# Optimization experiments

Hardware: AMD Instinct MI355X
Metric: run time of the kernel (lower is better)

Reference implementation:

```python
import jax, jax.numpy as jnp
import numpy as np

N_NODES = 100000
IN_CH = 256
OUT_CH = 128
N_EDGES = 3200000
SCALING_FACTOR = 1.8


def gcn_propagate(x, edge_index, num_nodes):
    """APPNP(K=1, alpha=0) == one step of D^-1/2 (A+I) D^-1/2 @ x."""
    row, col = edge_index[0], edge_index[1]
    loops = jnp.arange(num_nodes, dtype=edge_index.dtype)
    row = jnp.concatenate([row, loops])
    col = jnp.concatenate([col, loops])
    ones = jnp.ones(row.shape[0], dtype=x.dtype)
    deg = jax.ops.segment_sum(ones, col, num_segments=num_nodes)  # [N]
    dinv = jnp.where(deg > 0, jax.lax.rsqrt(deg), 0.0)
    norm = dinv[row] * dinv[col]  # [E+N]
    msgs = x[row] * norm[:, None]  # gather + scale, [E+N, C]
    return jax.ops.segment_sum(msgs, col, num_segments=num_nodes)  # [N, C]


def setup_inputs() -> dict:
    key = jax.random.key(0)
    ks = jax.random.split(key, 7)
    x = jax.random.normal(ks[0], (N_NODES, IN_CH), dtype=jnp.float32)
    edge_index = jax.random.randint(ks[1], (2, N_EDGES), 0, N_NODES, dtype=jnp.int64)
    s1 = 1.0 / np.sqrt(IN_CH)
    W1 = jax.random.uniform(ks[2], (IN_CH, OUT_CH), jnp.float32, -s1, s1)
    b1 = jax.random.uniform(ks[3], (OUT_CH,), jnp.float32, -s1, s1)
    W2 = jax.random.uniform(ks[4], (IN_CH, OUT_CH), jnp.float32, -s1, s1)
    b2 = jax.random.uniform(ks[5], (OUT_CH,), jnp.float32, -s1, s1)
    return {"x": x, "edge_index": edge_index, "W1": W1, "b1": b1, "W2": W2, "b2": b2}


def reference(x, edge_index, W1, b1, W2, b2):
    num_nodes = x.shape[0]
    # branch 1: linear1 then propagate
    x_ = x @ W1 + b1
    x_ = gcn_propagate(x_, edge_index, num_nodes)
    # branch 2: linear2, L2 normalize per-row, scale, then propagate
    h = x @ W2 + b2
    nrm = jnp.sqrt(jnp.sum(h * h, axis=1, keepdims=True))
    h = h / jnp.maximum(nrm, 1e-12) * SCALING_FACTOR
    h = gcn_propagate(h, edge_index, num_nodes)
    return (h, x_)
```

## Files before the change

### kernel.cpp

```cpp
#include <hip/hip_runtime.h>

#define IN_CH   256
#define OUT_CH  128
#define SCALE   1.8f
#define GT_M    32
#define BKT_SH  8
#define BKT_CAP 9216

using bf16x8 = __attribute__((ext_vector_type(8))) short;
using f32x4  = __attribute__((ext_vector_type(4))) float;

__device__ __forceinline__ float blo(unsigned int w) { return __uint_as_float(w << 16); }
__device__ __forceinline__ float bhi(unsigned int w) { return __uint_as_float(w & 0xffff0000u); }
__device__ __forceinline__ unsigned short f2b(float f) {
    unsigned int u = __float_as_uint(f);
    u += 0x7fffu + ((u >> 16) & 1u);
    return (unsigned short)(u >> 16);
}
__device__ __forceinline__ void split2(float f, unsigned short& h, unsigned short& l) {
    h = f2b(f);
    float hf = __uint_as_float((unsigned int)h << 16);
    l = f2b(f - hf);
}

__global__ __launch_bounds__(256) void wsplit_kernel(const float* __restrict__ W1, const float* __restrict__ b1,
                                                     const float* __restrict__ W2, const float* __restrict__ b2,
                                                     unsigned short* __restrict__ Wht, unsigned short* __restrict__ Wlt,
                                                     float* __restrict__ bc, int* __restrict__ bktCur) {
    int n = blockIdx.x;
    int k = threadIdx.x;
    if (n < 2) {
        int i = n * 256 + k;
        bktCur[i] = i * BKT_CAP;
    }
    float w = (n < OUT_CH) ? W2[k * OUT_CH + n] : W1[k * OUT_CH + (n - OUT_CH)];
    unsigned short h, l;
    split2(w, h, l);
    Wht[n * IN_CH + k] = h;
    Wlt[n * IN_CH + k] = l;
    if (k == 0) bc[n] = (n < OUT_CH) ? b2[n] : b1[n - OUT_CH];
}

__device__ __forceinline__ void part_body(char* smem, const int* __restrict__ row, const int* __restrict__ col,
                                          int* __restrict__ bktCur, unsigned int* __restrict__ pairs,
                                          int E, int NBKT, int nPart, int pb) {
    int* lh   = (int*)smem;
    int* lcur = lh + 512;
    int t = threadIdx.x;
    lh[t] = 0; lh[t + 256] = 0;
    __syncthreads();
    int tile = (E + nPart - 1) / nPart;
    int e0 = pb * tile;
    int e1 = min(E, e0 + tile);
    for (int i = e0 + t; i < e1; i += 256)
        atomicAdd(&lh[col[i] >> BKT_SH], 1);
    __syncthreads();
    for (int b = t; b < 512; b += 256) {
        int c = (b < NBKT) ? lh[b] : 0;
        lcur[b] = (c > 0) ? atomicAdd(&bktCur[b], c) : 0;
    }
    __syncthreads();
    for (int i = e0 + t; i < e1; i += 256) {
        int c = col[i];
        int b = c >> BKT_SH;
        int pos = atomicAdd(&lcur[b], 1);
        pairs[pos] = ((unsigned int)(c & 255) << 17) | (unsigned int)row[i];
    }
}

__device__ __forceinline__ void csr_body(char* smem, const unsigned int* __restrict__ pairs,
                                         const int* __restrict__ bktCur,
                                         int* __restrict__ csr, int* __restrict__ offs,
                                         int* __restrict__ deg, float* __restrict__ dinv,
                                         int N, int b) {
    int* s    = (int*)smem;
    int* nc   = (int*)(smem + 1024);
    int* ncur = (int*)(smem + 2048);
    int t = threadIdx.x;
    int base = b * BKT_CAP;
    int cnt = bktCur[b] - base;

    nc[t] = 0;
    __syncthreads();
    for (int i = t; i < cnt; i += 256)
        atomicAdd(&nc[pairs[base + i] >> 17], 1);
    __syncthreads();
    int dv = nc[t];
    s[t] = dv;
    __syncthreads();
    for (int o = 1; o < 256; o <<= 1) {
        int u = (t >= o) ? s[t - o] : 0;
        __syncthreads();
        s[t] += u;
        __syncthreads();
    }
    int rel = s[t] - dv;
    int n = (b << BKT_SH) + t;
    if (n < N) {
        offs[n] = base + rel;
        deg[n] = dv;
        dinv[n] = 1.0f / sqrtf((float)dv + 1.0f);
    }
    ncur[t] = rel;
    __syncthreads();
    for (int i = t; i < cnt; i += 256) {
        unsigned int k = pairs[base + i];
        int node = k >> 17;
        int pos = atomicAdd(&ncur[node], 1);
        csr[base + pos] = (int)(k & 0x1FFFF);
    }
}

#define XPAD 264
#define GEMM_SMEM (GT_M * XPAD * 2 + 2 * GT_M * 4)
__device__ __forceinline__ void gemm_body(char* smem, const float* __restrict__ x,
                                          const unsigned short* __restrict__ Wht,
                                          const unsigned short* __restrict__ Wlt,
                                          const float* __restrict__ bc,
                                          unsigned short* __restrict__ gb, int blockRow) {
    unsigned short* xh = (unsigned short*)smem;
    float* sn = (float*)(smem + GT_M * XPAD * sizeof(unsigned short));

    int t = threadIdx.x;
    size_t row0 = (size_t)blockRow * GT_M;

    const float4* xg = (const float4*)(x + row0 * IN_CH);
#pragma unroll
    for (int i = 0; i < 8; i++) {
        int f4 = t + i * 256;
        float4 v = xg[f4];
        int row = f4 >> 6;
        int c4 = (f4 & 63) * 4;
        uint2 hw;
        hw.x = (unsigned int)f2b(v.x) | ((unsigned int)f2b(v.y) << 16);
        hw.y = (unsigned int)f2b(v.z) | ((unsigned int)f2b(v.w) << 16);
        *(uint2*)&xh[row * XPAD + c4] = hw;
    }
    __syncthreads();

    int lane = t & 63;
    int wv = t >> 6;
    int lr = lane & 15;
    int lk = (lane >> 4) * 8;

    f32x4 acc[2][4];
#pragma unroll
    for (int rt = 0; rt < 2; rt++)
#pragma unroll
        for (int ct = 0; ct < 4; ct++) acc[rt][ct] = (f32x4){0.f, 0.f, 0.f, 0.f};

#pragma unroll
    for (int kt = 0; kt < 8; kt++) {
        int k0 = kt * 32;
        bf16x8 ah[2];
#pragma unroll
        for (int rt = 0; rt < 2; rt++) {
            int idx = (rt * 16 + lr) * XPAD + k0 + lk;
            ah[rt] = *(const bf16x8*)&xh[idx];
        }
        bf16x8 bh[4], bl[4];
#pragma unroll
        for (int ct = 0; ct < 4; ct++) {
            int n = wv * 64 + ct * 16 + lr;
            bh[ct] = *(const bf16x8*)&Wht[n * IN_CH + k0 + lk];
            bl[ct] = *(const bf16x8*)&Wlt[n * IN_CH + k0 + lk];
        }
#pragma unroll
        for (int rt = 0; rt < 2; rt++)
#pragma unroll
            for (int ct = 0; ct < 4; ct++) {
                acc[rt][ct] = __builtin_amdgcn_mfma_f32_16x16x32_bf16(ah[rt], bh[ct], acc[rt][ct], 0, 0, 0);
                acc[rt][ct] = __builtin_amdgcn_mfma_f32_16x16x32_bf16(ah[rt], bl[ct], acc[rt][ct], 0, 0, 0);
            }
    }
    __syncthreads();

    float bcv[4];
#pragma unroll
    for (int ct = 0; ct < 4; ct++) bcv[ct] = bc[wv * 64 + ct * 16 + lr];
#pragma unroll
    for (int rt = 0; rt < 2; rt++)
#pragma unroll
        for (int ct = 0; ct < 4; ct++)
#pragma unroll
            for (int j = 0; j < 4; j++) acc[rt][ct][j] += bcv[ct];

    if (wv < 2) {
        float nr[2][4];
#pragma unroll
        for (int rt = 0; rt < 2; rt++)
#pragma unroll
            for (int j = 0; j < 4; j++) {
                float sum = 0.f;
#pragma unroll
                for (int ct = 0; ct < 4; ct++) sum += acc[rt][ct][j] * acc[rt][ct][j];
                nr[rt][j] = sum;
            }
#pragma unroll
        for (int o = 1; o < 16; o <<= 1)
#pragma unroll
            for (int rt = 0; rt < 2; rt++)
#pragma unroll
                for (int j = 0; j < 4; j++) nr[rt][j] += __shfl_xor(nr[rt][j], o);
        if (lr == 0) {
#pragma unroll
            for (int rt = 0; rt < 2; rt++)
#pragma unroll
                for (int j = 0; j < 4; j++)
                    sn[wv * GT_M + rt * 16 + (lane >> 4) * 4 + j] = nr[rt][j];
        }
    }
    __syncthreads();

#pragma unroll
    for (int rt = 0; rt < 2; rt++) {
#pragma unroll
        for (int j = 0; j < 4; j++) {
            int rl = rt * 16 + (lane >> 4) * 4 + j;
            float sf;
            if (wv < 2) {
                float n2 = sn[rl] + sn[GT_M + rl];
                sf = SCALE / fmaxf(sqrtf(n2), 1e-12f);
            } else {
                sf = 1.0f;
            }
            size_t base = (row0 + rl) * 256;
#pragma unroll
            for (int ct = 0; ct < 4; ct++) {
                int col = wv * 64 + ct * 16 + lr;
                gb[base + col] = f2b(acc[rt][ct][j] * sf);
            }
        }
    }
}

__global__ __launch_bounds__(256) void k1_part_gemm(const int* __restrict__ row, const int* __restrict__ col,
                                                    int* __restrict__ bktCur, unsigned int* __restrict__ pairs,
                                                    int E, int NBKT, int nPart,
                                                    const float* __restrict__ x,
                                                    const unsigned short* __restrict__ Wht,
                                                    const unsigned short* __restrict__ Wlt,
                                                    const float* __restrict__ bc,
                                                    unsigned short* __restrict__ gb) {
    __shared__ __align__(16) char smem[GEMM_SMEM];
    int b = (int)blockIdx.x;
    if (b < nPart) part_body(smem, row, col, bktCur, pairs, E, NBKT, nPart, b);
    else gemm_body(smem, x, Wht, Wlt, bc, gb, b - nPart);
}

__global__ __launch_bounds__(256) void k2_csr_gemm(const unsigned int* __restrict__ pairs,
                                                   const int* __restrict__ bktCur,
                                                   int* __restrict__ csr, int* __restrict__ offs,
                                                   int* __restrict__ deg, float* __restrict__ dinv,
                                                   int N, int nCsr, int gemmRowBase,
                                                   const float* __restrict__ x,
                                                   const unsigned short* __restrict__ Wht,
                                                   const unsigned short* __restrict__ Wlt,
                                                   const float* __restrict__ bc,
                                                   unsigned short* __restrict__ gb) {
    __shared__ __align__(16) char smem[GEMM_SMEM];
    int b = (int)blockIdx.x;
    if (b < nCsr) csr_body(smem, pairs, bktCur, csr, offs, deg, dinv, N, b);
    else gemm_body(smem, x, Wht, Wlt, bc, gb, gemmRowBase + (b - nCsr));
}

__global__ __launch_bounds__(256) void gather_kernel(const uint4* __restrict__ gp,
                                                     const int* __restrict__ offs, const int* __restrict__ deg,
                                                     const int* __restrict__ csr, const float* __restrict__ dinv,
                                                     float* __restrict__ outh, float* __restrict__ outx, int N) {
    int t = threadIdx.x;
    int n = (blockIdx.x << 2) + (t >> 6);
    if (n >= N) return;
    int l = t & 63;
    int half = l >> 5;
    int cl = l & 31;

    float a0 = 0.f, a1 = 0.f, a2 = 0.f, a3 = 0.f, a4 = 0.f, a5 = 0.f, a6 = 0.f, a7 = 0.f;
    auto accumw = [&](uint4 w, float ds) {
        a0 += blo(w.x) * ds; a1 += bhi(w.x) * ds;
        a2 += blo(w.y) * ds; a3 += bhi(w.y) * ds;
        a4 += blo(w.z) * ds; a5 += bhi(w.z) * ds;
        a6 += blo(w.w) * ds; a7 += bhi(w.w) * ds;
    };

    float dn = dinv[n];
    if (half == 0) accumw(gp[(size_t)n * 32 + cl], dn);

    int s0 = offs[n];
    int e1 = s0 + deg[n];
    int e = s0 + half;
    for (; e + 2 < e1; e += 4) {
        int sa = csr[e];
        int sb = csr[e + 2];
        float da = dinv[sa];
        float db = dinv[sb];
        uint4 wa = gp[(size_t)sa * 32 + cl];
        uint4 wb = gp[(size_t)sb * 32 + cl];
        accumw(wa, da); accumw(wb, db);
    }
    for (; e < e1; e += 2) {
        int sa = csr[e];
        accumw(gp[(size_t)sa * 32 + cl], dinv[sa]);
    }

    a0 += __shfl_xor(a0, 32);
    a1 += __shfl_xor(a1, 32);
    a2 += __shfl_xor(a2, 32);
    a3 += __shfl_xor(a3, 32);
    a4 += __shfl_xor(a4, 32);
    a5 += __shfl_xor(a5, 32);
    a6 += __shfl_xor(a6, 32);
    a7 += __shfl_xor(a7, 32);

    if (half == 0) {
        float4 v0 = {a0 * dn, a1 * dn, a2 * dn, a3 * dn};
        float4 v1 = {a4 * dn, a5 * dn, a6 * dn, a7 * dn};
        if (cl < 16) {
            float* o = &outh[(size_t)n * OUT_CH + cl * 8];
            *(float4*)o = v0;
            *(float4*)(o + 4) = v1;
        } else {
            float* o = &outx[(size_t)n * OUT_CH + (cl - 16) * 8];
            *(float4*)o = v0;
            *(float4*)(o + 4) = v1;
        }
    }
}

extern "C" void kernel_launch(void* const* d_in, const int* in_sizes, int n_in,
                              void* d_out, int out_size, void* d_ws, size_t ws_size,
                              hipStream_t stream) {
    const float* x   = (const float*)d_in[0];
    const int*   ei  = (const int*)d_in[1];
    const float* W1  = (const float*)d_in[2];
    const float* b1  = (const float*)d_in[3];
    const float* W2  = (const float*)d_in[4];
    const float* b2  = (const float*)d_in[5];

    const int N = in_sizes[0] / IN_CH;
    const int E = in_sizes[1] / 2;
    const int NBKT = (N + 255) >> BKT_SH;

    float* outh = (float*)d_out;
    float* outx = outh + (size_t)N * OUT_CH;

    char* p = (char*)d_ws;
    auto take = [&](size_t bytes) {
        char* q = p;
        p += (bytes + 255) & ~(size_t)255;
        return q;
    };
    int*   deg     = (int*)take((size_t)N * sizeof(int));
    float* dinv    = (float*)take((size_t)N * sizeof(float));
    int*   offs    = (int*)take((size_t)N * sizeof(int));
    int*   bktCur  = (int*)take(512 * sizeof(int));
    float* bc      = (float*)take(256 * sizeof(float));
    unsigned short* Wht = (unsigned short*)take(256 * 256 * sizeof(unsigned short));
    unsigned short* Wlt = (unsigned short*)take(256 * 256 * sizeof(unsigned short));
    int*   csr     = (int*)take((size_t)NBKT * BKT_CAP * sizeof(int));
    unsigned int* pairs = (unsigned int*)take((size_t)NBKT * BKT_CAP * sizeof(unsigned int));
    unsigned short* gb = (unsigned short*)take((size_t)N * 256 * sizeof(unsigned short));

    const int* erow = ei;
    const int* ecol = ei + E;

    const int nPart = 512;
    const int gemmBlocks = N / GT_M;
    const int gemmA = (gemmBlocks + 1) / 2;
    const int gemmB = gemmBlocks - gemmA;

    wsplit_kernel<<<256, 256, 0, stream>>>(W1, b1, W2, b2, Wht, Wlt, bc, bktCur);
    k1_part_gemm<<<nPart + gemmA, 256, 0, stream>>>(erow, ecol, bktCur, pairs, E, NBKT, nPart,
                                                    x, Wht, Wlt, bc, gb);
    k2_csr_gemm<<<NBKT + gemmB, 256, 0, stream>>>(pairs, bktCur, csr, offs, deg, dinv, N, NBKT, gemmA,
                                                  x, Wht, Wlt, bc, gb);
    gather_kernel<<<(N + 3) / 4, 256, 0, stream>>>((const uint4*)gb, offs, deg, csr, dinv, outh, outx, N);
}
```

Measured before the change: 446.7 us.

## Double GEMM row tile and pre-swizzle weights into MFMA fragment layout

The GEMM tile grows from 32 to 64 rows per block, so each weight fragment loaded from global memory feeds twice as many MFMAs. The tail is handled with row bounds checks and a rounded-up block count. The weight split kernel now writes W in a fragment-major layout, so each lane's bf16x8 load is contiguous and coalesced across the wave. The larger tile raises register and LDS use and halves the number of GEMM blocks that overlap with the partition and CSR phases.

```diff
diff --git a/kernel.cpp b/kernel.cpp
--- a/kernel.cpp
+++ b/kernel.cpp
@@ -3,7 +3,7 @@
 #define IN_CH   256
 #define OUT_CH  128
 #define SCALE   1.8f
-#define GT_M    32
+#define GT_M    64
 #define BKT_SH  8
 #define BKT_CAP 9216
 
@@ -25,7 +25,7 @@
 
 __global__ __launch_bounds__(256) void wsplit_kernel(const float* __restrict__ W1, const float* __restrict__ b1,
                                                      const float* __restrict__ W2, const float* __restrict__ b2,
-                                                     unsigned short* __restrict__ Wht, unsigned short* __restrict__ Wlt,
+                                                     unsigned short* __restrict__ Wfh, unsigned short* __restrict__ Wfl,
                                                      float* __restrict__ bc, int* __restrict__ bktCur) {
     int n = blockIdx.x;
     int k = threadIdx.x;
@@ -36,8 +36,9 @@
     float w = (n < OUT_CH) ? W2[k * OUT_CH + n] : W1[k * OUT_CH + (n - OUT_CH)];
     unsigned short h, l;
     split2(w, h, l);
-    Wht[n * IN_CH + k] = h;
-    Wlt[n * IN_CH + k] = l;
+    int idx = (((k >> 5) * 16 + (n >> 4)) * 64 + ((k >> 3) & 3) * 16 + (n & 15)) * 8 + (k & 7);
+    Wfh[idx] = h;
+    Wfl[idx] = l;
     if (k == 0) bc[n] = (n < OUT_CH) ? b2[n] : b1[n - OUT_CH];
 }
 
@@ -114,10 +115,10 @@
 #define XPAD 264
 #define GEMM_SMEM (GT_M * XPAD * 2 + 2 * GT_M * 4)
 __device__ __forceinline__ void gemm_body(char* smem, const float* __restrict__ x,
-                                          const unsigned short* __restrict__ Wht,
-                                          const unsigned short* __restrict__ Wlt,
+                                          const unsigned short* __restrict__ Wfh,
+                                          const unsigned short* __restrict__ Wfl,
                                           const float* __restrict__ bc,
-                                          unsigned short* __restrict__ gb, int blockRow) {
+                                          unsigned short* __restrict__ gb, int blockRow, int N) {
     unsigned short* xh = (unsigned short*)smem;
     float* sn = (float*)(smem + GT_M * XPAD * sizeof(unsigned short));
 
@@ -126,14 +127,16 @@
 
     const float4* xg = (const float4*)(x + row0 * IN_CH);
 #pragma unroll
-    for (int i = 0; i < 8; i++) {
+    for (int i = 0; i < 16; i++) {
         int f4 = t + i * 256;
-        float4 v = xg[f4];
         int row = f4 >> 6;
         int c4 = (f4 & 63) * 4;
-        uint2 hw;
-        hw.x = (unsigned int)f2b(v.x) | ((unsigned int)f2b(v.y) << 16);
-        hw.y = (unsigned int)f2b(v.z) | ((unsigned int)f2b(v.w) << 16);
+        uint2 hw = {0u, 0u};
+        if (row0 + row < (size_t)N) {
+            float4 v = xg[f4];
+            hw.x = (unsigned int)f2b(v.x) | ((unsigned int)f2b(v.y) << 16);
+            hw.y = (unsigned int)f2b(v.z) | ((unsigned int)f2b(v.w) << 16);
+        }
         *(uint2*)&xh[row * XPAD + c4] = hw;
     }
     __syncthreads();
@@ -143,30 +146,30 @@
     int lr = lane & 15;
     int lk = (lane >> 4) * 8;
 
-    f32x4 acc[2][4];
-#pragma unroll
-    for (int rt = 0; rt < 2; rt++)
+    f32x4 acc[4][4];
+#pragma unroll
+    for (int rt = 0; rt < 4; rt++)
 #pragma unroll
         for (int ct = 0; ct < 4; ct++) acc[rt][ct] = (f32x4){0.f, 0.f, 0.f, 0.f};
 
 #pragma unroll
     for (int kt = 0; kt < 8; kt++) {
         int k0 = kt * 32;
-        bf16x8 ah[2];
-#pragma unroll
-        for (int rt = 0; rt < 2; rt++) {
+        bf16x8 bh[4], bl[4];
+#pragma unroll
+        for (int ct = 0; ct < 4; ct++) {
+            int fidx = ((kt * 16 + wv * 4 + ct) * 64 + lane) * 8;
+            bh[ct] = *(const bf16x8*)&Wfh[fidx];
+            bl[ct] = *(const bf16x8*)&Wfl[fidx];
+        }
+        bf16x8 ah[4];
+#pragma unroll
+        for (int rt = 0; rt < 4; rt++) {
             int idx = (rt * 16 + lr) * XPAD + k0 + lk;
             ah[rt] = *(const bf16x8*)&xh[idx];
         }
-        bf16x8 bh[4], bl[4];
-#pragma unroll
-        for (int ct = 0; ct < 4; ct++) {
-            int n = wv * 64 + ct * 16 + lr;
-            bh[ct] = *(const bf16x8*)&Wht[n * IN_CH + k0 + lk];
-            bl[ct] = *(const bf16x8*)&Wlt[n * IN_CH + k0 + lk];
-        }
-#pragma unroll
-        for (int rt = 0; rt < 2; rt++)
+#pragma unroll
+        for (int rt = 0; rt < 4; rt++)
 #pragma unroll
             for (int ct = 0; ct < 4; ct++) {
                 acc[rt][ct] = __builtin_amdgcn_mfma_f32_16x16x32_bf16(ah[rt], bh[ct], acc[rt][ct], 0, 0, 0);
@@ -179,16 +182,16 @@
 #pragma unroll
     for (int ct = 0; ct < 4; ct++) bcv[ct] = bc[wv * 64 + ct * 16 + lr];
 #pragma unroll
-    for (int rt = 0; rt < 2; rt++)
+    for (int rt = 0; rt < 4; rt++)
 #pragma unroll
         for (int ct = 0; ct < 4; ct++)
 #pragma unroll
             for (int j = 0; j < 4; j++) acc[rt][ct][j] += bcv[ct];
 
     if (wv < 2) {
-        float nr[2][4];
-#pragma unroll
-        for (int rt = 0; rt < 2; rt++)
+        float nr[4][4];
+#pragma unroll
+        for (int rt = 0; rt < 4; rt++)
 #pragma unroll
             for (int j = 0; j < 4; j++) {
                 float sum = 0.f;
@@ -199,12 +202,12 @@
 #pragma unroll
         for (int o = 1; o < 16; o <<= 1)
 #pragma unroll
-            for (int rt = 0; rt < 2; rt++)
+            for (int rt = 0; rt < 4; rt++)
 #pragma unroll
                 for (int j = 0; j < 4; j++) nr[rt][j] += __shfl_xor(nr[rt][j], o);
         if (lr == 0) {
 #pragma unroll
-            for (int rt = 0; rt < 2; rt++)
+            for (int rt = 0; rt < 4; rt++)
 #pragma unroll
                 for (int j = 0; j < 4; j++)
                     sn[wv * GT_M + rt * 16 + (lane >> 4) * 4 + j] = nr[rt][j];
@@ -213,10 +216,11 @@
     __syncthreads();
 
 #pragma unroll
-    for (int rt = 0; rt < 2; rt++) {
+    for (int rt = 0; rt < 4; rt++) {
 #pragma unroll
         for (int j = 0; j < 4; j++) {
             int rl = rt * 16 + (lane >> 4) * 4 + j;
+            if (row0 + rl >= (size_t)N) continue;
             float sf;
             if (wv < 2) {
                 float n2 = sn[rl] + sn[GT_M + rl];
@@ -238,14 +242,14 @@
                                                     int* __restrict__ bktCur, unsigned int* __restrict__ pairs,
                                                     int E, int NBKT, int nPart,
                                                     const float* __restrict__ x,
-                                                    const unsigned short* __restrict__ Wht,
-                                                    const unsigned short* __restrict__ Wlt,
+                                                    const unsigned short* __restrict__ Wfh,
+                                                    const unsigned short* __restrict__ Wfl,
                                                     const float* __restrict__ bc,
-                                                    unsigned short* __restrict__ gb) {
+                                                    unsigned short* __restrict__ gb, int N) {
     __shared__ __align__(16) char smem[GEMM_SMEM];
     int b = (int)blockIdx.x;
     if (b < nPart) part_body(smem, row, col, bktCur, pairs, E, NBKT, nPart, b);
-    else gemm_body(smem, x, Wht, Wlt, bc, gb, b - nPart);
+    else gemm_body(smem, x, Wfh, Wfl, bc, gb, b - nPart, N);
 }
 
 __global__ __launch_bounds__(256) void k2_csr_gemm(const unsigned int* __restrict__ pairs,
@@ -254,14 +258,14 @@
                                                    int* __restrict__ deg, float* __restrict__ dinv,
                                                    int N, int nCsr, int gemmRowBase,
                                                    const float* __restrict__ x,
-                                                   const unsigned short* __restrict__ Wht,
-                                                   const unsigned short* __restrict__ Wlt,
+                                                   const unsigned short* __restrict__ Wfh,
+                                                   const unsigned short* __restrict__ Wfl,
                                                    const float* __restrict__ bc,
                                                    unsigned short* __restrict__ gb) {
     __shared__ __align__(16) char smem[GEMM_SMEM];
     int b = (int)blockIdx.x;
     if (b < nCsr) csr_body(smem, pairs, bktCur, csr, offs, deg, dinv, N, b);
-    else gemm_body(smem, x, Wht, Wlt, bc, gb, gemmRowBase + (b - nCsr));
+    else gemm_body(smem, x, Wfh, Wfl, bc, gb, gemmRowBase + (b - nCsr), N);
 }
 
 __global__ __launch_bounds__(256) void gather_kernel(const uint4* __restrict__ gp,
@@ -355,8 +359,8 @@
     int*   offs    = (int*)take((size_t)N * sizeof(int));
     int*   bktCur  = (int*)take(512 * sizeof(int));
     float* bc      = (float*)take(256 * sizeof(float));
-    unsigned short* Wht = (unsigned short*)take(256 * 256 * sizeof(unsigned short));
-    unsigned short* Wlt = (unsigned short*)take(256 * 256 * sizeof(unsigned short));
+    unsigned short* Wfh = (unsigned short*)take(256 * 256 * sizeof(unsigned short));
+    unsigned short* Wfl = (unsigned short*)take(256 * 256 * sizeof(unsigned short));
     int*   csr     = (int*)take((size_t)NBKT * BKT_CAP * sizeof(int));
     unsigned int* pairs = (unsigned int*)take((size_t)NBKT * BKT_CAP * sizeof(unsigned int));
     unsigned short* gb = (unsigned short*)take((size_t)N * 256 * sizeof(unsigned short));
@@ -365,14 +369,14 @@
     const int* ecol = ei + E;
 
     const int nPart = 512;
-    const int gemmBlocks = N / GT_M;
+    const int gemmBlocks = (N + GT_M - 1) / GT_M;
     const int gemmA = (gemmBlocks + 1) / 2;
     const int gemmB = gemmBlocks - gemmA;
 
-    wsplit_kernel<<<256, 256, 0, stream>>>(W1, b1, W2, b2, Wht, Wlt, bc, bktCur);
+    wsplit_kernel<<<256, 256, 0, stream>>>(W1, b1, W2, b2, Wfh, Wfl, bc, bktCur);
     k1_part_gemm<<<nPart + gemmA, 256, 0, stream>>>(erow, ecol, bktCur, pairs, E, NBKT, nPart,
-                                                    x, Wht, Wlt, bc, gb);
+                                                    x, Wfh, Wfl, bc, gb, N);
     k2_csr_gemm<<<NBKT + gemmB, 256, 0, stream>>>(pairs, bktCur, csr, offs, deg, dinv, N, NBKT, gemmA,
-                                                  x, Wht, Wlt, bc, gb);
+                                                  x, Wfh, Wfl, bc, gb);
     gather_kernel<<<(N + 3) / 4, 256, 0, stream>>>((const uint4*)gb, offs, deg, csr, dinv, outh, outx, N);
 }
```

Result: faster. 401.8 us (-10.1%).
